# Performance work log

Measured on AMD Instinct MI355X. Metric: run time of the kernel, lower is better.

The kernel has to match this reference:

```python
import jax, jax.numpy as jnp
import numpy as np

L, B, T, D, H, F, V = 4, 2, 1024, 1024, 16, 4096, 32000
DH = D // H
POWER = 4
EPS = 1e-6


def _anorm(x, gain):
    # y = g * x / (mean(|x|) + eps)  (L1 'diamond' norm)
    return gain * (x / (jnp.mean(jnp.abs(x), axis=-1, keepdims=True) + EPS))


def _rational_softmax(x):
    s = x / (jnp.abs(x) + 1.0)          # squash to (-1, 1)
    p = ((s + 1.0) * 0.5) ** POWER      # shift to (0,1), sharpen
    return p / (jnp.sum(p, axis=-1, keepdims=True) + EPS)


def setup_inputs() -> dict:
    key = jax.random.key(0)
    ks = jax.random.split(key, 12)
    w = 0.02  # weight scale for stability
    return {
        "idx": jax.random.randint(ks[0], (B, T), 0, V),
        "tok_emb": jax.random.normal(ks[1], (V, D), jnp.float32) * w,
        "pos_emb": jax.random.normal(ks[2], (T, D), jnp.float32) * w,
        "Wq": jax.random.normal(ks[3], (L, D, D), jnp.float32) * w,
        "bq": jnp.zeros((L, D), jnp.float32),
        "Wk": jax.random.normal(ks[4], (L, D, D), jnp.float32) * w,
        "bk": jnp.zeros((L, D), jnp.float32),
        "Wv": jax.random.normal(ks[5], (L, D, D), jnp.float32) * w,
        "bv": jnp.zeros((L, D), jnp.float32),
        "Wo": jax.random.normal(ks[6], (L, D, D), jnp.float32) * w,
        "bo": jnp.zeros((L, D), jnp.float32),
        "score_gain": jnp.full((L,), 4.0, jnp.float32),
        "norm1_gain": jnp.ones((L, D), jnp.float32),
        "norm2_gain": jnp.ones((L, D), jnp.float32),
        "W1": jax.random.normal(ks[7], (L, D, F), jnp.float32) * w,
        "b1": jnp.zeros((L, F), jnp.float32),
        "W2": jax.random.normal(ks[8], (L, F, D), jnp.float32) * w,
        "b2": jnp.zeros((L, D), jnp.float32),
        "final_gain": jnp.ones((D,), jnp.float32),
        "Wlm": jax.random.normal(ks[9], (D, V), jnp.float32) * w,
        "blm": jnp.zeros((V,), jnp.float32),
    }


def _forward(idx, tok_emb, pos_emb, Wq, bq, Wk, bk, Wv, bv, Wo, bo,
             score_gain, norm1_gain, norm2_gain, W1, b1, W2, b2,
             final_gain, Wlm, blm):
    Bx, Tx = idx.shape
    x = tok_emb[idx] + pos_emb[:Tx]                 # [B,T,D]
    mask = jnp.triu(jnp.ones((Tx, Tx), bool), 1)    # causal mask (True = masked)
    for l in range(L):
        # --- algebraic attention ---
        h = _anorm(x, norm1_gain[l])
        q = (h @ Wq[l] + bq[l]).reshape(Bx, Tx, H, DH).transpose(0, 2, 1, 3)
        k = (h @ Wk[l] + bk[l]).reshape(Bx, Tx, H, DH).transpose(0, 2, 1, 3)
        v = (h @ Wv[l] + bv[l]).reshape(Bx, Tx, H, DH).transpose(0, 2, 1, 3)
        scores = jnp.einsum('bhqd,bhkd->bhqk', q, k)
        scores = scores - jnp.mean(scores, axis=-1, keepdims=True)
        mad = jnp.mean(jnp.abs(scores), axis=-1, keepdims=True) + EPS
        scores = (scores / mad) * score_gain[l]
        scores = jnp.where(mask, -1000.0, scores)
        attn = _rational_softmax(scores)
        o = jnp.einsum('bhqk,bhkd->bhqd', attn, v)
        o = o.transpose(0, 2, 1, 3).reshape(Bx, Tx, D)
        x = x + (o @ Wo[l] + bo[l])
        # --- FFN with algebraic ReLU ---
        h = _anorm(x, norm2_gain[l])
        h = jnp.maximum(h @ W1[l] + b1[l], 0.0)
        x = x + (h @ W2[l] + b2[l])
    x = _anorm(x, final_gain)
    return x @ Wlm + blm                            # [B,T,V] logits


def reference(idx, tok_emb, pos_emb, Wq, bq, Wk, bk, Wv, bv, Wo, bo,
              score_gain, norm1_gain, norm2_gain, W1, b1, W2, b2,
              final_gain, Wlm, blm):
    return _forward(idx, tok_emb, pos_emb, Wq, bq, Wk, bk, Wv, bv, Wo, bo,
                    score_gain, norm1_gain, norm2_gain, W1, b1, W2, b2,
                    final_gain, Wlm, blm)
```

## Files before the change

### kernel.cpp

```cpp
#include <hip/hip_runtime.h>

typedef unsigned short u16;
typedef __bf16 bf16x8 __attribute__((ext_vector_type(8)));
typedef float f32x4 __attribute__((ext_vector_type(4)));
typedef unsigned int u32;

#define EPSF 1e-6f

__device__ __forceinline__ u16 f2bf(float f) {
  union { float f; unsigned u; } un; un.f = f;
  unsigned r = un.u + 0x7FFFu + ((un.u >> 16) & 1u);
  return (u16)(r >> 16);
}

__device__ __forceinline__ float block_sum(float v) {
  #pragma unroll
  for (int off = 32; off > 0; off >>= 1) v += __shfl_xor(v, off, 64);
  __shared__ float ws[4];
  const int w = threadIdx.x >> 6;
  __syncthreads();
  if ((threadIdx.x & 63) == 0) ws[w] = v;
  __syncthreads();
  return ws[0] + ws[1] + ws[2] + ws[3];
}

__device__ __forceinline__ void lds_cp16(const void* g, void* l) {
  __builtin_amdgcn_global_load_lds(
      (__attribute__((address_space(1))) void*)g,
      (__attribute__((address_space(3))) void*)l, 16, 0, 0);
}

__global__ __launch_bounds__(256) void embed_norm(
    const int* __restrict__ idx, const float* __restrict__ tok,
    const float* __restrict__ pos, const float* __restrict__ gain,
    float* __restrict__ x, u16* __restrict__ h) {
  const int row = blockIdx.x;
  const int tpos = row & 1023;
  const int token = idx[row];
  const int d = threadIdx.x * 4;
  const float4 a = *(const float4*)(tok + (long)token * 1024 + d);
  const float4 b = *(const float4*)(pos + (long)tpos * 1024 + d);
  float4 o; o.x = a.x + b.x; o.y = a.y + b.y; o.z = a.z + b.z; o.w = a.w + b.w;
  *(float4*)(x + (long)row * 1024 + d) = o;
  float s = fabsf(o.x) + fabsf(o.y) + fabsf(o.z) + fabsf(o.w);
  s = block_sum(s);
  const float scale = 1.0f / (s * (1.0f / 1024.0f) + EPSF);
  const float4 g = *(const float4*)(gain + d);
  ushort4 ov;
  ov.x = f2bf(o.x * g.x * scale);
  ov.y = f2bf(o.y * g.y * scale);
  ov.z = f2bf(o.z * g.z * scale);
  ov.w = f2bf(o.w * g.w * scale);
  *(ushort4*)(h + (long)row * 1024 + d) = ov;
}

__global__ __launch_bounds__(512, 4) void attn_v5(
    const u16* __restrict__ qkv, const u16* __restrict__ v_t,
    u16* __restrict__ obuf, const float* __restrict__ score_gain, int l) {
  __shared__ float red1[2][4][16], red2[2][4][16], red3[2][4][16];
  __shared__ float Ured[2][4][16][68];
  __shared__ u16 Pl[8][640];
  const int qt = blockIdx.x, h = blockIdx.y, b = blockIdx.z;
  const int tid = threadIdx.x, w = tid >> 6, l64 = tid & 63;
  const int lq = l64 & 15, kgrp = l64 >> 4;
  const int wq = w >> 2, tq = w & 3;
  const int qglob = qt * 32 + wq * 16 + lq;
  const int qmax  = qt * 32 + wq * 16 + 15;
  const u16* Qg = qkv + (size_t)b * (1024 * 3072) + h * 64;
  const u16* Kg = Qg + 1024;
  const u16* Vt = v_t + (size_t)(b * 16 + h) * (64 * 1024);
  char* Pw = (char*)&Pl[w][0];

  bf16x8 qB0, qB1;
  {
    const u16* qp = Qg + (size_t)qglob * 3072 + (kgrp << 3);
    qB0 = *(const bf16x8*)qp;
    qB1 = *(const bf16x8*)(qp + 32);
  }

  f32x4 s[16];
  {
    const u16* Ktq = Kg + (size_t)(tq * 32 + lq) * 3072 + (kgrp << 3);
    #pragma unroll
    for (int tl = 0; tl < 16; tl++) {
      const int cst = ((tl >> 1) << 7) + ((tl & 1) << 4);
      const u16* kp = Ktq + (size_t)cst * 3072;
      const bf16x8 k0 = *(const bf16x8*)kp;
      const bf16x8 k1 = *(const bf16x8*)(kp + 32);
      f32x4 d = {0.f, 0.f, 0.f, 0.f};
      d = __builtin_amdgcn_mfma_f32_16x16x32_bf16(k0, qB0, d, 0, 0, 0);
      d = __builtin_amdgcn_mfma_f32_16x16x32_bf16(k1, qB1, d, 0, 0, 0);
      s[tl] = d;
    }
  }

  float ssum = 0.f;
  #pragma unroll
  for (int tl = 0; tl < 16; tl++)
    ssum += (s[tl][0] + s[tl][1]) + (s[tl][2] + s[tl][3]);
  ssum += __shfl_xor(ssum, 16, 64);
  ssum += __shfl_xor(ssum, 32, 64);
  if (l64 < 16) red1[wq][tq][l64] = ssum;
  __syncthreads();
  const float mean = (red1[wq][0][lq] + red1[wq][1][lq] +
                      red1[wq][2][lq] + red1[wq][3][lq]) * (1.0f / 1024.0f);

  float asum = 0.f;
  #pragma unroll
  for (int tl = 0; tl < 16; tl++)
    asum += fabsf(s[tl][0] - mean) + fabsf(s[tl][1] - mean) +
            fabsf(s[tl][2] - mean) + fabsf(s[tl][3] - mean);
  asum += __shfl_xor(asum, 16, 64);
  asum += __shfl_xor(asum, 32, 64);
  if (l64 < 16) red2[wq][tq][l64] = asum;
  __syncthreads();
  const float mad = (red2[wq][0][lq] + red2[wq][1][lq] +
                     red2[wq][2][lq] + red2[wq][3][lq]) * (1.0f / 1024.0f) + EPSF;
  const float gs = score_gain[l] / mad;

  float psum = 0.f;
  #pragma unroll
  for (int tl = 0; tl < 16; tl++) {
    const int tbase = tq * 32 + ((tl >> 1) << 7) + ((tl & 1) << 4);
    #pragma unroll
    for (int j = 0; j < 4; j++) {
      const int t = tbase + (kgrp << 2) + j;
      float sv = (s[tl][j] - mean) * gs;
      if (t > qglob) sv = -1000.0f;
      const float rr = sv / (fabsf(sv) + 1.0f);
      const float a1 = (rr + 1.0f) * 0.5f;
      const float a2 = a1 * a1;
      s[tl][j] = a2 * a2;
      psum += s[tl][j];
    }
  }

  f32x4 U[4] = {};
  {
    const u16* Vtq = Vt + (size_t)lq * 1024 + tq * 32 + (kgrp << 3);
    #pragma unroll
    for (int cc = 0; cc < 8; cc++) {
      const int t0 = tq * 32 + (cc << 7);
      if (t0 <= qmax) {
        bf16x8 vA[4];
        #pragma unroll
        for (int dt = 0; dt < 4; dt++)
          vA[dt] = *(const bf16x8*)(Vtq + (size_t)(dt << 4) * 1024 + (cc << 7));
        #pragma unroll
        for (int half = 0; half < 2; half++) {
          #pragma unroll
          for (int pr = 0; pr < 2; pr++) {
            const u32 pk = (u32)f2bf(s[2 * cc + half][pr * 2]) |
                           ((u32)f2bf(s[2 * cc + half][pr * 2 + 1]) << 16);
            *(u32*)(Pw + lq * 80 + half * 32 + (kgrp << 3) + (pr << 2)) = pk;
          }
        }
        asm volatile("s_waitcnt lgkmcnt(0)" ::: "memory");
        __builtin_amdgcn_sched_barrier(0);
        const bf16x8 pB = *(const bf16x8*)(Pw + lq * 80 + (kgrp << 4));
        #pragma unroll
        for (int dt = 0; dt < 4; dt++)
          U[dt] = __builtin_amdgcn_mfma_f32_16x16x32_bf16(vA[dt], pB, U[dt], 0, 0, 0);
      }
    }
  }

  psum += __shfl_xor(psum, 16, 64);
  psum += __shfl_xor(psum, 32, 64);
  if (l64 < 16) red3[wq][tq][l64] = psum;
  #pragma unroll
  for (int dt = 0; dt < 4; dt++)
    *(float4*)&Ured[wq][tq][lq][(dt << 4) + (kgrp << 2)] = *(const float4*)&U[dt];
  __syncthreads();

  {
    const int qq = tid >> 4, dhseg = (tid & 15) << 2;
    const int fwq = qq >> 4, flq = qq & 15;
    const float fps = red3[fwq][0][flq] + red3[fwq][1][flq] +
                      red3[fwq][2][flq] + red3[fwq][3][flq];
    const float oinv = 1.0f / (fps + EPSF);
    float4 u0 = *(const float4*)&Ured[fwq][0][flq][dhseg];
    const float4 u1 = *(const float4*)&Ured[fwq][1][flq][dhseg];
    const float4 u2 = *(const float4*)&Ured[fwq][2][flq][dhseg];
    const float4 u3 = *(const float4*)&Ured[fwq][3][flq][dhseg];
    u0.x = (u0.x + u1.x + u2.x + u3.x) * oinv;
    u0.y = (u0.y + u1.y + u2.y + u3.y) * oinv;
    u0.z = (u0.z + u1.z + u2.z + u3.z) * oinv;
    u0.w = (u0.w + u1.w + u2.w + u3.w) * oinv;
    ushort4 o;
    o.x = f2bf(u0.x); o.y = f2bf(u0.y); o.z = f2bf(u0.z); o.w = f2bf(u0.w);
    u16* dst = obuf + ((size_t)((b << 10) + qt * 32 + qq) << 10) + (h << 6) + dhseg;
    *(ushort4*)dst = o;
  }
}

__global__ void wconv_all(
    const float* __restrict__ Wq, const float* __restrict__ Wk,
    const float* __restrict__ Wv, const float* __restrict__ Wo,
    const float* __restrict__ W1, const float* __restrict__ W2,
    const float* __restrict__ Wlm,
    u16* __restrict__ wqkv_t, u16* __restrict__ wo_t,
    u16* __restrict__ w1_t, u16* __restrict__ w2_t, u16* __restrict__ wlm_t) {
  __shared__ float tile[64][65];
  const int bid = blockIdx.x;
  const float* src; u16* dst; int R, C, c0, r0;
  if (bid < 4096) {
    const int l = bid >> 10, m = (bid >> 8) & 3, t = bid & 255;
    if (m == 0)      src = Wq + (size_t)l * 1048576;
    else if (m == 1) src = Wk + (size_t)l * 1048576;
    else if (m == 2) src = Wv + (size_t)l * 1048576;
    else             src = Wo + (size_t)l * 1048576;
    dst = (m < 3) ? wqkv_t + ((size_t)l * 3072 + m * 1024) * 1024
                  : wo_t + (size_t)l * 1048576;
    R = 1024; C = 1024; c0 = (t & 15) << 6; r0 = (t >> 4) << 6;
  } else if (bid < 8192) {
    const int i = bid - 4096, l = i >> 10, t = i & 1023;
    src = W1 + (size_t)l * 4194304; dst = w1_t + (size_t)l * 4194304;
    R = 1024; C = 4096; c0 = (t & 63) << 6; r0 = (t >> 6) << 6;
  } else if (bid < 12288) {
    const int i = bid - 8192, l = i >> 10, t = i & 1023;
    src = W2 + (size_t)l * 4194304; dst = w2_t + (size_t)l * 4194304;
    R = 4096; C = 1024; c0 = (t & 15) << 6; r0 = (t >> 4) << 6;
  } else {
    const int i = bid - 12288;
    src = Wlm; dst = wlm_t;
    R = 1024; C = 32000; c0 = (i % 500) << 6; r0 = (i / 500) << 6;
  }
  const int tx = threadIdx.x, ty = threadIdx.y;
  const int cg = (tx & 15) << 2;
  const int rg = tx >> 4;
  #pragma unroll
  for (int i = 0; i < 4; i++) {
    const int row = i * 16 + ty * 4 + rg;
    const float4 v = *(const float4*)&src[(long)(r0 + row) * C + c0 + cg];
    tile[row][cg] = v.x; tile[row][cg + 1] = v.y;
    tile[row][cg + 2] = v.z; tile[row][cg + 3] = v.w;
  }
  __syncthreads();
  #pragma unroll
  for (int i = 0; i < 4; i++) {
    const int c = i * 16 + ty * 4 + rg;
    ushort4 o;
    o.x = f2bf(tile[cg][c]);     o.y = f2bf(tile[cg + 1][c]);
    o.z = f2bf(tile[cg + 2][c]); o.w = f2bf(tile[cg + 3][c]);
    *(ushort4*)&dst[(long)(c0 + c) * R + r0 + cg] = o;
  }
}

__global__ __launch_bounds__(256) void bias_concat(
    const float* __restrict__ bq, const float* __restrict__ bk,
    const float* __restrict__ bv, float* __restrict__ out) {
  const int i = blockIdx.x * 256 + threadIdx.x;
  const int l = i / 3072, j = i % 3072;
  float v;
  if (j < 1024)      v = bq[l * 1024 + j];
  else if (j < 2048) v = bk[l * 1024 + j - 1024];
  else               v = bv[l * 1024 + j - 2048];
  out[i] = v;
}

template <int NPART>
__global__ __launch_bounds__(256) void reduce_norm(
    const float* __restrict__ part, const float* __restrict__ bias,
    float* __restrict__ x, const float* __restrict__ gain,
    u16* __restrict__ h) {
  const int row = blockIdx.x, c = threadIdx.x * 4;
  float4 acc = *(const float4*)(part + (size_t)row * 1024 + c);
  #pragma unroll
  for (int i = 1; i < NPART; i++) {
    const float4 pi = *(const float4*)(part + (size_t)(row + i * 2048) * 1024 + c);
    acc.x += pi.x; acc.y += pi.y; acc.z += pi.z; acc.w += pi.w;
  }
  const float4 bb = *(const float4*)(bias + c);
  float4 xv = *(float4*)(x + (size_t)row * 1024 + c);
  xv.x += acc.x + bb.x;
  xv.y += acc.y + bb.y;
  xv.z += acc.z + bb.z;
  xv.w += acc.w + bb.w;
  *(float4*)(x + (size_t)row * 1024 + c) = xv;
  float s = fabsf(xv.x) + fabsf(xv.y) + fabsf(xv.z) + fabsf(xv.w);
  s = block_sum(s);
  const float scale = 1.0f / (s * (1.0f / 1024.0f) + EPSF);
  const float4 g = *(const float4*)(gain + c);
  ushort4 o;
  o.x = f2bf(xv.x * g.x * scale);
  o.y = f2bf(xv.y * g.y * scale);
  o.z = f2bf(xv.z * g.z * scale);
  o.w = f2bf(xv.w * g.w * scale);
  *(ushort4*)(h + (size_t)row * 1024 + c) = o;
}

template <bool OUT_BF16, bool BIAS, bool RELU, bool RESID>
__global__ __launch_bounds__(512) void gemm256_kernel(
    const u16* __restrict__ A, long lda,
    const u16* __restrict__ Bt, long ldb,
    void* __restrict__ Cv, long ldc,
    const float* __restrict__ bias, const float* __restrict__ resid,
    int M, int N, int K, int nTM) {
  __shared__ u16 lds[65536];
  const int nwg = gridDim.x;
  const int qx = nwg >> 3, rx = nwg & 7;
  const int xcd = blockIdx.x & 7, seq = blockIdx.x >> 3;
  const int wg = (xcd < rx ? xcd * (qx + 1) : rx * (qx + 1) + (xcd - rx) * qx) + seq;
  const int tm = wg % nTM, tn = wg / nTM;
  const int rowA0 = tm * 256, rowB0 = tn * 256;

  const int t = threadIdx.x, w = t >> 6, l = t & 63;
  const int lrow = l & 15, kgrp = l >> 4;
  const int wr = w >> 2, wc = w & 3;

  const int srow = t >> 2;
  const int scol = ((t & 3) ^ ((t >> 3) & 3)) * 8;
  const u16* Asrc = A + (long)(rowA0 + srow) * lda + scol;
  const u16* Bsrc = Bt + (long)(rowB0 + srow) * ldb + scol;
  char* ldsB = (char*)lds;
  const int wbase = w * 1024;

  const int fswz = (kgrp ^ ((lrow >> 1) & 3)) * 8;
  const int aoff = (wr * 128 + lrow) * 32 + fswz;
  const int boff = 8192 + (wc * 64 + lrow) * 32 + fswz;

  f32x4 acc[8][4] = {};
  const int NT = K >> 5;

  #pragma unroll
  for (int pt = 0; pt < 3; pt++) {
    const int k0 = pt << 5;
    const int bb = pt * 32768;
    lds_cp16(Asrc + k0,                    ldsB + bb + wbase);
    lds_cp16(Asrc + (long)128 * lda + k0,  ldsB + bb + 8192 + wbase);
    lds_cp16(Bsrc + k0,                    ldsB + bb + 16384 + wbase);
    lds_cp16(Bsrc + (long)128 * ldb + k0,  ldsB + bb + 24576 + wbase);
  }

  for (int tt = 0; tt < NT; tt++) {
    const int rem = NT - 1 - tt;
    if (rem >= 2)      asm volatile("s_waitcnt vmcnt(8)" ::: "memory");
    else if (rem == 1) asm volatile("s_waitcnt vmcnt(4)" ::: "memory");
    else               asm volatile("s_waitcnt vmcnt(0)" ::: "memory");
    __builtin_amdgcn_sched_barrier(0);
    __builtin_amdgcn_s_barrier();

    const u16* buf = lds + (tt & 3) * 16384;
    const int stage = tt + 3 < NT;
    const int k0n = (tt + 3) << 5;
    const int bbn = ((tt + 3) & 3) * 32768;

    bf16x8 aF[4], bF[4];
    #pragma unroll
    for (int m = 0; m < 4; m++) aF[m] = *(const bf16x8*)(buf + aoff + m * 512);
    #pragma unroll
    for (int n = 0; n < 4; n++) bF[n] = *(const bf16x8*)(buf + boff + n * 512);
    if (stage) {
      lds_cp16(Asrc + k0n,                   ldsB + bbn + wbase);
      lds_cp16(Asrc + (long)128 * lda + k0n, ldsB + bbn + 8192 + wbase);
    }
    asm volatile("s_waitcnt lgkmcnt(0)" ::: "memory");
    __builtin_amdgcn_sched_barrier(0);
    __builtin_amdgcn_s_setprio(1);
    #pragma unroll
    for (int m = 0; m < 4; m++)
      #pragma unroll
      for (int n = 0; n < 4; n++)
        acc[m][n] = __builtin_amdgcn_mfma_f32_16x16x32_bf16(aF[m], bF[n], acc[m][n], 0, 0, 0);
    __builtin_amdgcn_s_setprio(0);

    #pragma unroll
    for (int m = 0; m < 4; m++) aF[m] = *(const bf16x8*)(buf + aoff + (m + 4) * 512);
    if (stage) {
      lds_cp16(Bsrc + k0n,                   ldsB + bbn + 16384 + wbase);
      lds_cp16(Bsrc + (long)128 * ldb + k0n, ldsB + bbn + 24576 + wbase);
    }
    asm volatile("s_waitcnt lgkmcnt(0)" ::: "memory");
    __builtin_amdgcn_sched_barrier(0);
    __builtin_amdgcn_s_setprio(1);
    #pragma unroll
    for (int m = 0; m < 4; m++)
      #pragma unroll
      for (int n = 0; n < 4; n++)
        acc[m + 4][n] = __builtin_amdgcn_mfma_f32_16x16x32_bf16(aF[m], bF[n], acc[m + 4][n], 0, 0, 0);
    __builtin_amdgcn_s_setprio(0);
  }

  float bvv[4];
  #pragma unroll
  for (int n = 0; n < 4; n++)
    bvv[n] = BIAS ? bias[rowB0 + wc * 64 + n * 16 + lrow] : 0.0f;
  #pragma unroll
  for (int m = 0; m < 8; m++) {
    const int row = rowA0 + wr * 128 + m * 16 + kgrp * 4;
    #pragma unroll
    for (int n = 0; n < 4; n++) {
      const int col = rowB0 + wc * 64 + n * 16 + lrow;
      #pragma unroll
      for (int j = 0; j < 4; j++) {
        float v = acc[m][n][j] + bvv[n];
        if (RELU) v = fmaxf(v, 0.0f);
        const long off = (long)(row + j) * ldc + col;
        if (RESID) v += resid[off];
        if (OUT_BF16) ((u16*)Cv)[off] = f2bf(v);
        else          ((float*)Cv)[off] = v;
      }
    }
  }
}

template <bool OUT_BF16, bool BIAS, bool RELU, bool RESID, bool VTOUT>
__global__ __launch_bounds__(256) void gemm128p(
    const u16* __restrict__ A, long lda, long sA,
    const u16* __restrict__ Bt, long ldb, long sB,
    void* __restrict__ Cv, long ldc, long sC,
    const float* __restrict__ bias, const float* __restrict__ resid,
    u16* __restrict__ vtout,
    int M, int N, int K, int nTM) {
  __shared__ u16 lds[32768];
  const int nwg = gridDim.x;
  const int qx = nwg >> 3, rx = nwg & 7;
  const int xcd = blockIdx.x & 7, seq = blockIdx.x >> 3;
  const int wg = (xcd < rx ? xcd * (qx + 1) : rx * (qx + 1) + (xcd - rx) * qx) + seq;
  const int tm = wg % nTM, tn = wg / nTM;
  const int batch = blockIdx.y;
  A  += (long)batch * sA;
  Bt += (long)batch * sB;
  const int rowA0 = tm * 128, rowB0 = tn * 128;
  const int t = threadIdx.x, w = t >> 6, l = t & 63;
  const int lrow = l & 15, kgrp = l >> 4;
  const int wr = (w >> 1) << 6, wc = (w & 1) << 6;

  const int srow = t >> 2;
  const int scol = ((t & 3) ^ ((t >> 3) & 3)) * 8;
  const u16* Asrc = A + (long)(rowA0 + srow) * lda + scol;
  const u16* Bsrc = Bt + (long)(rowB0 + srow) * ldb + scol;
  char* ldsB = (char*)lds;
  const int wbase = w * 1024;

  const int swz8 = (kgrp ^ ((lrow >> 1) & 3)) * 8;
  const int aoff = (wr + lrow) * 32 + swz8;
  const int boff = 4096 + (wc + lrow) * 32 + swz8;

  f32x4 acc[4][4] = {};
  const int NT = K >> 5;

  #pragma unroll
  for (int pt = 0; pt < 3; pt++) {
    const int k0 = pt << 5;
    const int bb = pt * 16384;
    lds_cp16(Asrc + k0,                   ldsB + bb + wbase);
    lds_cp16(Asrc + (long)64 * lda + k0,  ldsB + bb + 4096 + wbase);
    lds_cp16(Bsrc + k0,                   ldsB + bb + 8192 + wbase);
    lds_cp16(Bsrc + (long)64 * ldb + k0,  ldsB + bb + 12288 + wbase);
  }

  for (int tt = 0; tt < NT; tt++) {
    const int rem = NT - 1 - tt;
    if (rem >= 2)      asm volatile("s_waitcnt vmcnt(8)" ::: "memory");
    else if (rem == 1) asm volatile("s_waitcnt vmcnt(4)" ::: "memory");
    else               asm volatile("s_waitcnt vmcnt(0)" ::: "memory");
    __builtin_amdgcn_sched_barrier(0);
    __builtin_amdgcn_s_barrier();

    const u16* buf = lds + (tt & 3) * 8192;
    const int stage = tt + 3 < NT;
    const int k0n = (tt + 3) << 5;
    const int bbn = ((tt + 3) & 3) * 16384;

    bf16x8 aF[4], bF[4];
    #pragma unroll
    for (int m = 0; m < 4; m++) aF[m] = *(const bf16x8*)(buf + aoff + m * 512);
    #pragma unroll
    for (int n = 0; n < 4; n++) bF[n] = *(const bf16x8*)(buf + boff + n * 512);
    if (stage) {
      lds_cp16(Asrc + k0n,                  ldsB + bbn + wbase);
      lds_cp16(Asrc + (long)64 * lda + k0n, ldsB + bbn + 4096 + wbase);
      lds_cp16(Bsrc + k0n,                  ldsB + bbn + 8192 + wbase);
      lds_cp16(Bsrc + (long)64 * ldb + k0n, ldsB + bbn + 12288 + wbase);
    }
    asm volatile("s_waitcnt lgkmcnt(0)" ::: "memory");
    __builtin_amdgcn_sched_barrier(0);
    __builtin_amdgcn_s_setprio(1);
    #pragma unroll
    for (int m = 0; m < 4; m++)
      #pragma unroll
      for (int n = 0; n < 4; n++)
        acc[m][n] = __builtin_amdgcn_mfma_f32_16x16x32_bf16(aF[m], bF[n], acc[m][n], 0, 0, 0);
    __builtin_amdgcn_s_setprio(0);
  }

  if (VTOUT && rowB0 >= 2048) {
    __syncthreads();
    #pragma unroll
    for (int m = 0; m < 4; m++) {
      #pragma unroll
      for (int n = 0; n < 4; n++) {
        const int c = wc + n * 16 + lrow;
        const int r = wr + m * 16 + (kgrp << 2);
        ushort4 pk;
        float v0 = acc[m][n][0], v1 = acc[m][n][1], v2 = acc[m][n][2], v3 = acc[m][n][3];
        if (BIAS) {
          const float bv = bias[rowB0 + c];
          v0 += bv; v1 += bv; v2 += bv; v3 += bv;
        }
        pk.x = f2bf(v0); pk.y = f2bf(v1); pk.z = f2bf(v2); pk.w = f2bf(v3);
        *(ushort4*)&lds[c * 136 + r] = pk;
      }
    }
    __syncthreads();
    {
      const int c = t >> 1, half = t & 1;
      const int dh = c & 63;
      const int h = ((rowB0 - 2048) >> 6) + (c >> 6);
      const int bb2 = rowA0 >> 10, t0 = rowA0 & 1023;
      u16* dst = vtout + (((size_t)(bb2 * 16 + h)) << 16) + ((size_t)dh << 10) +
                 t0 + half * 64;
      #pragma unroll
      for (int k = 0; k < 8; k++)
        *(bf16x8*)(dst + k * 8) = *(const bf16x8*)&lds[c * 136 + half * 64 + k * 8];
    }
  } else {
    const long coff = (long)batch * sC;
    #pragma unroll
    for (int m = 0; m < 4; m++) {
      #pragma unroll
      for (int n = 0; n < 4; n++) {
        const int col = rowB0 + wc + n * 16 + lrow;
        #pragma unroll
        for (int j = 0; j < 4; j++) {
          const int row = rowA0 + wr + m * 16 + (kgrp << 2) + j;
          float v = acc[m][n][j];
          if (BIAS) v += bias[col];
          if (RELU) v = fmaxf(v, 0.0f);
          const long off = coff + (long)row * ldc + col;
          if (RESID) v += resid[off];
          if (OUT_BF16) ((u16*)Cv)[off] = f2bf(v);
          else          ((float*)Cv)[off] = v;
        }
      }
    }
  }
}

extern "C" void kernel_launch(void* const* d_in, const int* in_sizes, int n_in,
                              void* d_out, int out_size, void* d_ws, size_t ws_size,
                              hipStream_t stream) {
  constexpr int Lc = 4, Tc = 1024, Dc = 1024, Hc = 16, Fc = 4096, DHc = 64;
  const int M = 2 * Tc;

  const int*   idxp       = (const int*)  d_in[0];
  const float* tok_emb    = (const float*)d_in[1];
  const float* pos_emb    = (const float*)d_in[2];
  const float* Wq         = (const float*)d_in[3];
  const float* bq         = (const float*)d_in[4];
  const float* Wk         = (const float*)d_in[5];
  const float* bk         = (const float*)d_in[6];
  const float* Wv         = (const float*)d_in[7];
  const float* bv         = (const float*)d_in[8];
  const float* Wo         = (const float*)d_in[9];
  const float* bo         = (const float*)d_in[10];
  const float* score_gain = (const float*)d_in[11];
  const float* norm1_gain = (const float*)d_in[12];
  const float* norm2_gain = (const float*)d_in[13];
  const float* W1         = (const float*)d_in[14];
  const float* b1         = (const float*)d_in[15];
  const float* W2         = (const float*)d_in[16];
  const float* b2         = (const float*)d_in[17];
  const float* final_gain = (const float*)d_in[18];
  const float* Wlm        = (const float*)d_in[19];
  const float* blm        = (const float*)d_in[20];

  char* p = (char*)d_ws;
  auto alloc = [&](size_t n) { char* r = p; p += (n + 255) & ~(size_t)255; return r; };
  u16*  wqkv_t = (u16*) alloc((size_t)Lc * 3072 * 1024 * 2);
  u16*  wo_t   = (u16*) alloc((size_t)Lc * 1024 * 1024 * 2);
  u16*  w1_t   = (u16*) alloc((size_t)Lc * 4096 * 1024 * 2);
  u16*  w2_t   = (u16*) alloc((size_t)Lc * 1024 * 4096 * 2);
  u16*  wlm_t  = (u16*) alloc((size_t)32000 * 1024 * 2);
  float* bqkv  = (float*)alloc((size_t)Lc * 3072 * 4);
  float* x     = (float*)alloc((size_t)M * 1024 * 4);
  u16*  hbuf   = (u16*) alloc((size_t)M * 1024 * 2);
  u16*  qkv    = (u16*) alloc((size_t)M * 3072 * 2);
  u16*  v_t    = (u16*) alloc((size_t)2 * Hc * DHc * Tc * 2);
  u16*  obuf   = (u16*) alloc((size_t)M * 1024 * 2);
  u16*  ffh    = (u16*) alloc((size_t)M * 4096 * 2);
  float* fpart = (float*)alloc((size_t)4 * M * 1024 * 4);

  wconv_all<<<20288, dim3(64, 4), 0, stream>>>(Wq, Wk, Wv, Wo, W1, W2, Wlm,
                                               wqkv_t, wo_t, w1_t, w2_t, wlm_t);
  bias_concat<<<48, 256, 0, stream>>>(bq, bk, bv, bqkv);
  embed_norm<<<M, 256, 0, stream>>>(idxp, tok_emb, pos_emb, norm1_gain, x, hbuf);

  for (int l = 0; l < Lc; l++) {
    gemm128p<true, true, false, false, true><<<dim3(16 * 24, 1), 256, 0, stream>>>(
        hbuf, 1024, 0, wqkv_t + (size_t)l * 3072 * 1024, 1024, 0,
        qkv, 3072, 0, bqkv + (size_t)l * 3072, nullptr, v_t, M, 3072, 1024, 16);

    attn_v5<<<dim3(32, 16, 2), 512, 0, stream>>>(qkv, v_t, obuf, score_gain, l);

    gemm128p<false, false, false, false, false><<<dim3(128, 2), 256, 0, stream>>>(
        obuf, 1024, 512, wo_t + (size_t)l * 1024 * 1024, 1024, 512,
        fpart, 1024, (long)M * 1024, nullptr, nullptr, nullptr, M, 1024, 512, 16);
    reduce_norm<2><<<M, 256, 0, stream>>>(fpart, bo + (size_t)l * Dc, x,
                                          norm2_gain + (size_t)l * Dc, hbuf);
    gemm128p<true, true, true, false, false><<<dim3(16 * 32, 1), 256, 0, stream>>>(
        hbuf, 1024, 0, w1_t + (size_t)l * Fc * Dc, 1024, 0,
        ffh, 4096, 0, b1 + (size_t)l * Fc, nullptr, nullptr, M, 4096, 1024, 16);
    gemm128p<false, false, false, false, false><<<dim3(128, 4), 256, 0, stream>>>(
        ffh, 4096, 1024, w2_t + (size_t)l * Dc * Fc, 4096, 1024,
        fpart, 1024, (long)M * 1024, nullptr, nullptr, nullptr, M, 1024, 1024, 16);
    const float* gnext = (l < Lc - 1) ? (norm1_gain + (size_t)(l + 1) * Dc) : final_gain;
    reduce_norm<4><<<M, 256, 0, stream>>>(fpart, b2 + (size_t)l * Dc, x, gnext, hbuf);
  }

  gemm256_kernel<false, true, false, false><<<dim3(1000), 512, 0, stream>>>(
      hbuf, 1024, wlm_t, 1024,
      d_out, 32000, blm, nullptr, M, 32000, 1024, 8);
}
```

Measured before the change: 978.9 us.

## Restructure LM-head GEMM to double-buffered BK=64 with interleaved staging

Replaces the LM-head 256x256 GEMM main loop, which used a 4-stage ring of K=32 slices, with two 64-wide K buffers. The new loop interleaves four MFMA groups with split LDS reads and global-to-LDS staging, and uses a new 8-way swizzle on 128-byte rows. The goal is fewer barriers per unit of K and better overlap of loads with MFMA work on the largest GEMM. The cost is more register pressure from six fragment arrays and only two stages of prefetch depth. Unused RELU and RESID template paths are removed.

```diff
diff --git a/kernel.cpp b/kernel.cpp
--- a/kernel.cpp
+++ b/kernel.cpp
@@ -290,12 +290,12 @@
   *(ushort4*)(h + (size_t)row * 1024 + c) = o;
 }
 
-template <bool OUT_BF16, bool BIAS, bool RELU, bool RESID>
-__global__ __launch_bounds__(512) void gemm256_kernel(
+template <bool OUT_BF16, bool BIAS>
+__global__ __launch_bounds__(512) void gemm256_8p(
     const u16* __restrict__ A, long lda,
     const u16* __restrict__ Bt, long ldb,
     void* __restrict__ Cv, long ldc,
-    const float* __restrict__ bias, const float* __restrict__ resid,
+    const float* __restrict__ bias,
     int M, int N, int K, int nTM) {
   __shared__ u16 lds[65536];
   const int nwg = gridDim.x;
@@ -309,77 +309,122 @@
   const int lrow = l & 15, kgrp = l >> 4;
   const int wr = w >> 2, wc = w & 3;
 
-  const int srow = t >> 2;
-  const int scol = ((t & 3) ^ ((t >> 3) & 3)) * 8;
-  const u16* Asrc = A + (long)(rowA0 + srow) * lda + scol;
-  const u16* Bsrc = Bt + (long)(rowB0 + srow) * ldb + scol;
+  const int srow = (w << 3) + (l >> 3);
+  const int scol = (((l & 7) ^ (l >> 3)) << 3);
+  const u16* Ab = A + (long)rowA0 * lda;
+  const u16* Bb = Bt + (long)rowB0 * ldb;
   char* ldsB = (char*)lds;
-  const int wbase = w * 1024;
-
-  const int fswz = (kgrp ^ ((lrow >> 1) & 3)) * 8;
-  const int aoff = (wr * 128 + lrow) * 32 + fswz;
-  const int boff = 8192 + (wc * 64 + lrow) * 32 + fswz;
+  const int wb = w << 10;
+
+  auto stg = [&](int db, int region, int q, int k0) {
+    const u16* srcb = region ? Bb : Ab;
+    const long ld = region ? ldb : lda;
+    lds_cp16(srcb + (long)(q * 64 + srow) * ld + k0 + scol,
+             ldsB + db * 65536 + region * 32768 + q * 8192 + wb);
+  };
+
+  const int aswz = lrow & 7;
+  const int kc0 = (kgrp ^ aswz) << 4;
+  const int kc1 = ((4 + kgrp) ^ aswz) << 4;
+  int arow[8], brow[4];
+  #pragma unroll
+  for (int m = 0; m < 8; m++) arow[m] = (wr * 128 + m * 16 + lrow) * 128;
+  #pragma unroll
+  for (int n = 0; n < 4; n++) brow[n] = 32768 + (wc * 64 + n * 16 + lrow) * 128;
 
   f32x4 acc[8][4] = {};
-  const int NT = K >> 5;
-
-  #pragma unroll
-  for (int pt = 0; pt < 3; pt++) {
-    const int k0 = pt << 5;
-    const int bb = pt * 32768;
-    lds_cp16(Asrc + k0,                    ldsB + bb + wbase);
-    lds_cp16(Asrc + (long)128 * lda + k0,  ldsB + bb + 8192 + wbase);
-    lds_cp16(Bsrc + k0,                    ldsB + bb + 16384 + wbase);
-    lds_cp16(Bsrc + (long)128 * ldb + k0,  ldsB + bb + 24576 + wbase);
-  }
-
-  for (int tt = 0; tt < NT; tt++) {
-    const int rem = NT - 1 - tt;
-    if (rem >= 2)      asm volatile("s_waitcnt vmcnt(8)" ::: "memory");
-    else if (rem == 1) asm volatile("s_waitcnt vmcnt(4)" ::: "memory");
-    else               asm volatile("s_waitcnt vmcnt(0)" ::: "memory");
-    __builtin_amdgcn_sched_barrier(0);
-    __builtin_amdgcn_s_barrier();
-
-    const u16* buf = lds + (tt & 3) * 16384;
-    const int stage = tt + 3 < NT;
-    const int k0n = (tt + 3) << 5;
-    const int bbn = ((tt + 3) & 3) * 32768;
-
-    bf16x8 aF[4], bF[4];
-    #pragma unroll
-    for (int m = 0; m < 4; m++) aF[m] = *(const bf16x8*)(buf + aoff + m * 512);
-    #pragma unroll
-    for (int n = 0; n < 4; n++) bF[n] = *(const bf16x8*)(buf + boff + n * 512);
-    if (stage) {
-      lds_cp16(Asrc + k0n,                   ldsB + bbn + wbase);
-      lds_cp16(Asrc + (long)128 * lda + k0n, ldsB + bbn + 8192 + wbase);
-    }
-    asm volatile("s_waitcnt lgkmcnt(0)" ::: "memory");
-    __builtin_amdgcn_sched_barrier(0);
-    __builtin_amdgcn_s_setprio(1);
-    #pragma unroll
-    for (int m = 0; m < 4; m++)
-      #pragma unroll
-      for (int n = 0; n < 4; n++)
-        acc[m][n] = __builtin_amdgcn_mfma_f32_16x16x32_bf16(aF[m], bF[n], acc[m][n], 0, 0, 0);
-    __builtin_amdgcn_s_setprio(0);
-
-    #pragma unroll
-    for (int m = 0; m < 4; m++) aF[m] = *(const bf16x8*)(buf + aoff + (m + 4) * 512);
-    if (stage) {
-      lds_cp16(Bsrc + k0n,                   ldsB + bbn + 16384 + wbase);
-      lds_cp16(Bsrc + (long)128 * ldb + k0n, ldsB + bbn + 24576 + wbase);
-    }
-    asm volatile("s_waitcnt lgkmcnt(0)" ::: "memory");
-    __builtin_amdgcn_sched_barrier(0);
-    __builtin_amdgcn_s_setprio(1);
-    #pragma unroll
-    for (int m = 0; m < 4; m++)
-      #pragma unroll
-      for (int n = 0; n < 4; n++)
-        acc[m + 4][n] = __builtin_amdgcn_mfma_f32_16x16x32_bf16(aF[m], bF[n], acc[m + 4][n], 0, 0, 0);
-    __builtin_amdgcn_s_setprio(0);
+  const int NKT = K >> 6;
+  const int NIT = NKT >> 1;
+
+  #pragma unroll
+  for (int q = 0; q < 4; q++) stg(0, 0, q, 0);
+  #pragma unroll
+  for (int q = 0; q < 4; q++) stg(0, 1, q, 0);
+  #pragma unroll
+  for (int q = 0; q < 4; q++) stg(1, 0, q, 64);
+  #pragma unroll
+  for (int q = 0; q < 4; q++) stg(1, 1, q, 64);
+
+  for (int it = 0; it < NIT; ++it) {
+    const int kt = it << 1;
+    const bool sok = (it < NIT - 1);
+    const int k2 = (kt + 2) << 6, k3 = (kt + 3) << 6;
+    bf16x8 a0[4], ah0[4], b0[4], a1[4], ah1[4], b1[4];
+
+    #pragma unroll
+    for (int half = 0; half < 2; half++) {
+      const int dbB = half * 65536;
+      const int kn = half ? k3 : k2;
+
+      if (half == 0 || sok) asm volatile("s_waitcnt vmcnt(8)" ::: "memory");
+      else                  asm volatile("s_waitcnt vmcnt(0)" ::: "memory");
+      __builtin_amdgcn_sched_barrier(0);
+      __builtin_amdgcn_s_barrier();
+
+      #pragma unroll
+      for (int m = 0; m < 4; m++) a0[m]  = *(const bf16x8*)(ldsB + dbB + arow[m] + kc0);
+      #pragma unroll
+      for (int n = 0; n < 4; n++) b0[n]  = *(const bf16x8*)(ldsB + dbB + brow[n] + kc0);
+      #pragma unroll
+      for (int m = 0; m < 4; m++) ah0[m] = *(const bf16x8*)(ldsB + dbB + arow[m + 4] + kc0);
+      asm volatile("s_waitcnt lgkmcnt(4)" ::: "memory");
+      __builtin_amdgcn_sched_barrier(0);
+      __builtin_amdgcn_s_setprio(1);
+      #pragma unroll
+      for (int m = 0; m < 4; m++)
+        #pragma unroll
+        for (int n = 0; n < 4; n++)
+          acc[m][n] = __builtin_amdgcn_mfma_f32_16x16x32_bf16(a0[m], b0[n], acc[m][n], 0, 0, 0);
+      __builtin_amdgcn_s_setprio(0);
+      __builtin_amdgcn_sched_barrier(0);
+
+      #pragma unroll
+      for (int m = 0; m < 4; m++) a1[m]  = *(const bf16x8*)(ldsB + dbB + arow[m] + kc1);
+      #pragma unroll
+      for (int n = 0; n < 4; n++) b1[n]  = *(const bf16x8*)(ldsB + dbB + brow[n] + kc1);
+      #pragma unroll
+      for (int m = 0; m < 4; m++) ah1[m] = *(const bf16x8*)(ldsB + dbB + arow[m + 4] + kc1);
+      asm volatile("s_waitcnt lgkmcnt(12)" ::: "memory");
+      __builtin_amdgcn_sched_barrier(0);
+      __builtin_amdgcn_s_setprio(1);
+      #pragma unroll
+      for (int m = 0; m < 4; m++)
+        #pragma unroll
+        for (int n = 0; n < 4; n++)
+          acc[m + 4][n] = __builtin_amdgcn_mfma_f32_16x16x32_bf16(ah0[m], b0[n], acc[m + 4][n], 0, 0, 0);
+      __builtin_amdgcn_s_setprio(0);
+      asm volatile("s_waitcnt lgkmcnt(0)" ::: "memory");
+      __builtin_amdgcn_sched_barrier(0);
+      __builtin_amdgcn_s_barrier();
+
+      if (sok) {
+        #pragma unroll
+        for (int q = 0; q < 4; q++) stg(half, 0, q, kn);
+      }
+      __builtin_amdgcn_sched_barrier(0);
+      __builtin_amdgcn_s_setprio(1);
+      #pragma unroll
+      for (int m = 0; m < 4; m++)
+        #pragma unroll
+        for (int n = 0; n < 4; n++)
+          acc[m][n] = __builtin_amdgcn_mfma_f32_16x16x32_bf16(a1[m], b1[n], acc[m][n], 0, 0, 0);
+      __builtin_amdgcn_s_setprio(0);
+      __builtin_amdgcn_sched_barrier(0);
+
+      if (sok) {
+        #pragma unroll
+        for (int q = 0; q < 4; q++) stg(half, 1, q, kn);
+      }
+      __builtin_amdgcn_sched_barrier(0);
+      __builtin_amdgcn_s_setprio(1);
+      #pragma unroll
+      for (int m = 0; m < 4; m++)
+        #pragma unroll
+        for (int n = 0; n < 4; n++)
+          acc[m + 4][n] = __builtin_amdgcn_mfma_f32_16x16x32_bf16(ah1[m], b1[n], acc[m + 4][n], 0, 0, 0);
+      __builtin_amdgcn_s_setprio(0);
+      __builtin_amdgcn_sched_barrier(0);
+    }
   }
 
   float bvv[4];
@@ -395,9 +440,7 @@
       #pragma unroll
       for (int j = 0; j < 4; j++) {
         float v = acc[m][n][j] + bvv[n];
-        if (RELU) v = fmaxf(v, 0.0f);
         const long off = (long)(row + j) * ldc + col;
-        if (RESID) v += resid[off];
         if (OUT_BF16) ((u16*)Cv)[off] = f2bf(v);
         else          ((float*)Cv)[off] = v;
       }
@@ -610,7 +653,7 @@
     reduce_norm<4><<<M, 256, 0, stream>>>(fpart, b2 + (size_t)l * Dc, x, gnext, hbuf);
   }
 
-  gemm256_kernel<false, true, false, false><<<dim3(1000), 512, 0, stream>>>(
+  gemm256_8p<false, true><<<dim3(1000), 512, 0, stream>>>(
       hbuf, 1024, wlm_t, 1024,
-      d_out, 32000, blm, nullptr, M, 32000, 1024, 8);
-}
+      d_out, 32000, blm, M, 32000, 1024, 8);
+}
```

Measured after the change: 1.150 ms. +17.4%, slower.
